# Optimization experiments

Measured on AMD Instinct MI355X. Metric: run time of the kernel, lower is better.

Reference implementation:

```python
import jax, jax.numpy as jnp
import numpy as np

N = 8192


def _bcsoftmax1d(x, c):
    # sort ascending by log(budget) - logit, as in the torch reference
    order = jnp.argsort(jnp.log(c) - x)
    xs, cs = x[order], c[order]
    # reversed log-cumsum-exp: log_r[i] = logsumexp(xs[i:])
    log_r = jnp.flip(jax.lax.cumlogsumexp(jnp.flip(xs)))
    # s[i] = 1 - sum_{j<i} cs[j]
    s = 1.0 - (jnp.cumsum(cs) - cs)
    in_kb = (cs == 0) | ((s - cs > 0) & (xs - log_r + jnp.log(s) > jnp.log(cs)))
    mask = ~in_kb
    m = jnp.max(jnp.where(mask, xs, -jnp.inf))
    exp_x = jnp.exp(xs - m)
    s2 = 1.0 - jnp.sum(cs * in_kb)
    r = jnp.sum(exp_x * mask)
    ys = jnp.where(mask, s2 * exp_x / r, cs)
    # undo the sort
    return jnp.zeros_like(ys).at[order].set(ys)


def setup_inputs() -> dict:
    key = jax.random.key(0)
    k1, k2, k3, k4 = jax.random.split(key, 4)
    x = jax.random.normal(k1, (N,), dtype=jnp.float32)
    # budgets must be > 0; scale so sum(c) ~ 1 so constraints can bind
    c = jax.random.uniform(k2, (N,), dtype=jnp.float32) * (2.0 / N)
    W = jax.random.normal(k3, (N, N), dtype=jnp.float32) / np.sqrt(N).astype(np.float32)
    b = jax.random.normal(k4, (N,), dtype=jnp.float32) * 0.01
    return {"x": x, "c": c, "W": W, "b": b}


def reference(x, c, W, b):
    h = W @ x + b  # nn.Linear: x @ W^T + b == W @ x for 1D x
    return _bcsoftmax1d(h, c)
```

## Files before the change

### kernel.cpp

```cpp
#include <hip/hip_runtime.h>
#include <math.h>

#define N 8192
typedef unsigned long long u64;

#define CE(a, b, d) do { if (((a) > (b)) == (d)) { u64 _t = (a); (a) = (b); (b) = _t; } } while (0)

__global__ __launch_bounds__(256) void matvec_k(const float* __restrict__ W,
                                                const float* __restrict__ x,
                                                const float* __restrict__ b,
                                                float* __restrict__ h) {
  const int lane = threadIdx.x & 63;
  const int row = blockIdx.x * 4 + (threadIdx.x >> 6);
  const float4* Wr = reinterpret_cast<const float4*>(W + (size_t)row * N);
  const float4* x4 = reinterpret_cast<const float4*>(x);
  float acc = 0.f;
#pragma unroll 8
  for (int k = 0; k < 32; ++k) {
    const int i = k * 64 + lane;
    const float4 w = Wr[i];
    const float4 xv = x4[i];
    acc = fmaf(w.x, xv.x, acc);
    acc = fmaf(w.y, xv.y, acc);
    acc = fmaf(w.z, xv.z, acc);
    acc = fmaf(w.w, xv.w, acc);
  }
#pragma unroll
  for (int off = 32; off > 0; off >>= 1) acc += __shfl_down(acc, off, 64);
  if (lane == 0) h[row] = acc + b[row];
}

__global__ __launch_bounds__(1024) void bcsoftmax_k(const float* __restrict__ h,
                                                    const float* __restrict__ c,
                                                    float* __restrict__ out) {
  __shared__ u64 sb[N];
  __shared__ float red[32];
  __shared__ float bcast[4];
  const int tid = threadIdx.x;
  const int lane = tid & 63;
  const int wid = tid >> 6;

  u64 v[8];

  float hv[8], cv[8];
  {
    const float4* h4 = reinterpret_cast<const float4*>(h);
    const float4* c4 = reinterpret_cast<const float4*>(c);
    const float4 a0 = h4[tid * 2], a1 = h4[tid * 2 + 1];
    const float4 b0 = c4[tid * 2], b1 = c4[tid * 2 + 1];
    hv[0] = a0.x; hv[1] = a0.y; hv[2] = a0.z; hv[3] = a0.w;
    hv[4] = a1.x; hv[5] = a1.y; hv[6] = a1.z; hv[7] = a1.w;
    cv[0] = b0.x; cv[1] = b0.y; cv[2] = b0.z; cv[3] = b0.w;
    cv[4] = b1.x; cv[5] = b1.y; cv[6] = b1.z; cv[7] = b1.w;
  }
  float lmax = -INFINITY;
#pragma unroll
  for (int p = 0; p < 8; ++p) {
    const int g = tid * 8 + p;
    const float key = logf(cv[p]) - hv[p];
    unsigned int u = __float_as_uint(key);
    u = (u & 0x80000000u) ? ~u : (u | 0x80000000u);
    v[p] = ((u64)u << 32) | (unsigned int)g;
    lmax = fmaxf(lmax, hv[p]);
  }
  CE(v[0], v[1], true); CE(v[2], v[3], false); CE(v[4], v[5], true); CE(v[6], v[7], false);
  CE(v[0], v[2], true); CE(v[1], v[3], true); CE(v[4], v[6], false); CE(v[5], v[7], false);
  CE(v[0], v[1], true); CE(v[2], v[3], true); CE(v[4], v[5], false); CE(v[6], v[7], false);
  {
    const bool d8 = ((tid & 1) == 0);
    CE(v[0], v[4], d8); CE(v[1], v[5], d8); CE(v[2], v[6], d8); CE(v[3], v[7], d8);
    CE(v[0], v[2], d8); CE(v[1], v[3], d8); CE(v[4], v[6], d8); CE(v[5], v[7], d8);
    CE(v[0], v[1], d8); CE(v[2], v[3], d8); CE(v[4], v[5], d8); CE(v[6], v[7], d8);
  }
#pragma unroll
  for (int p = 0; p < 8; ++p) sb[tid * 8 + p] = v[p];

#pragma unroll
  for (int off = 32; off > 0; off >>= 1) lmax = fmaxf(lmax, __shfl_down(lmax, off, 64));
  if (lane == 0) red[wid] = lmax;
  __syncthreads();
  if (tid == 0) {
    float mm = red[0];
    for (int i = 1; i < 16; ++i) mm = fmaxf(mm, red[i]);
    bcast[0] = mm;
  }

  for (int k = 16;; k <<= 1) {
    for (int j = k >> 1; j >= 8; j >>= 1) {
#pragma unroll
      for (int rep = 0; rep < 4; ++rep) {
        const int i = rep * 1024 + tid;
        const int t = ((i & ~(j - 1)) << 1) | (i & (j - 1));
        const int p = t | j;
        const u64 a = sb[t];
        const u64 bb = sb[p];
        const bool asc = ((t & k) == 0);
        if ((a > bb) == asc) { sb[t] = bb; sb[p] = a; }
      }
      __syncthreads();
    }
#pragma unroll
    for (int p = 0; p < 8; ++p) v[p] = sb[tid * 8 + p];
    const bool d = (((tid * 8) & k) == 0);
    CE(v[0], v[4], d); CE(v[1], v[5], d); CE(v[2], v[6], d); CE(v[3], v[7], d);
    CE(v[0], v[2], d); CE(v[1], v[3], d); CE(v[4], v[6], d); CE(v[5], v[7], d);
    CE(v[0], v[1], d); CE(v[2], v[3], d); CE(v[4], v[5], d); CE(v[6], v[7], d);
    if (k == N) break;
#pragma unroll
    for (int p = 0; p < 8; ++p) sb[tid * 8 + p] = v[p];
    __syncthreads();
  }

  const float M = bcast[0];
  int idx[8];
  float xs[8], cs[8], e[8];
  float cloc = 0.f, eloc = 0.f;
#pragma unroll
  for (int p = 0; p < 8; ++p) {
    const int id = (int)(v[p] & 0xFFFFFFFFull);
    idx[p] = id;
    xs[p] = h[id];
    cs[p] = c[id];
  }
#pragma unroll
  for (int p = 0; p < 8; ++p) {
    e[p] = expf(xs[p] - M);
    cloc += cs[p];
    eloc += e[p];
  }

  float cinc = cloc;
#pragma unroll
  for (int off = 1; off < 64; off <<= 1) {
    const float t = __shfl_up(cinc, off, 64);
    if (lane >= off) cinc += t;
  }
  float cwex = __shfl_up(cinc, 1, 64);
  if (lane == 0) cwex = 0.f;
  __syncthreads();
  if (lane == 63) red[wid] = cinc;
  __syncthreads();
  if (tid < 16) {
    float winc = red[tid];
#pragma unroll
    for (int off = 1; off < 16; off <<= 1) {
      const float t = __shfl_up(winc, off, 64);
      if (lane >= off) winc += t;
    }
    float wexc = __shfl_up(winc, 1, 64);
    if (tid == 0) wexc = 0.f;
    red[tid] = wexc;
  }
  __syncthreads();
  const float cthread_excl = red[wid] + cwex;

  float sinc = eloc;
#pragma unroll
  for (int off = 1; off < 64; off <<= 1) {
    const float t = __shfl_down(sinc, off, 64);
    if (lane + off < 64) sinc += t;
  }
  float swex = __shfl_down(sinc, 1, 64);
  if (lane == 63) swex = 0.f;
  __syncthreads();
  if (lane == 0) red[16 + wid] = sinc;
  __syncthreads();
  if (tid < 16) {
    float winc = red[16 + tid];
#pragma unroll
    for (int off = 1; off < 16; off <<= 1) {
      const float t = __shfl_down(winc, off, 64);
      if (tid + off < 16) winc += t;
    }
    float wexc = __shfl_down(winc, 1, 64);
    if (tid == 15) wexc = 0.f;
    red[16 + tid] = wexc;
  }
  __syncthreads();
  const float ethread_exsuf = red[16 + wid] + swex;

  float lsuf[8];
  lsuf[7] = e[7];
#pragma unroll
  for (int p = 6; p >= 0; --p) lsuf[p] = e[p] + lsuf[p + 1];
  float cexc = 0.f;
  bool kb[8];
  float lm = -INFINITY, lkbc = 0.f;
#pragma unroll
  for (int p = 0; p < 8; ++p) {
    const float s = 1.0f - (cthread_excl + cexc);
    const float suff = ethread_exsuf + lsuf[p];
    const float log_r = M + logf(suff);
    const bool in_kb =
        (cs[p] == 0.0f) ||
        ((s - cs[p] > 0.0f) && (xs[p] - log_r + logf(s) > logf(cs[p])));
    kb[p] = in_kb;
    if (in_kb) lkbc += cs[p];
    else       lm = fmaxf(lm, xs[p]);
    cexc += cs[p];
  }
#pragma unroll
  for (int off = 32; off > 0; off >>= 1) {
    lm = fmaxf(lm, __shfl_down(lm, off, 64));
    lkbc += __shfl_down(lkbc, off, 64);
  }
  __syncthreads();
  if (lane == 0) { red[wid] = lm; red[16 + wid] = lkbc; }
  __syncthreads();
  if (tid == 0) {
    float mm = red[0], sc = red[16];
    for (int i = 1; i < 16; ++i) { mm = fmaxf(mm, red[i]); sc += red[16 + i]; }
    bcast[1] = mm;
    bcast[2] = 1.0f - sc;
  }
  __syncthreads();
  const float m = bcast[1];
  const float s2 = bcast[2];

  float lr = 0.f;
#pragma unroll
  for (int p = 0; p < 8; ++p)
    if (!kb[p]) lr += expf(xs[p] - m);
#pragma unroll
  for (int off = 32; off > 0; off >>= 1) lr += __shfl_down(lr, off, 64);
  if (lane == 0) red[wid] = lr;
  __syncthreads();
  if (tid == 0) {
    float rr = red[0];
    for (int i = 1; i < 16; ++i) rr += red[i];
    bcast[3] = rr;
  }
  __syncthreads();
  const float r = bcast[3];

#pragma unroll
  for (int p = 0; p < 8; ++p) {
    out[idx[p]] = kb[p] ? cs[p] : s2 * expf(xs[p] - m) / r;
  }
}

extern "C" void kernel_launch(void* const* d_in, const int* in_sizes, int n_in,
                              void* d_out, int out_size, void* d_ws, size_t ws_size,
                              hipStream_t stream) {
  (void)in_sizes; (void)n_in; (void)out_size;
  const float* x = (const float*)d_in[0];
  const float* c = (const float*)d_in[1];
  const float* W = (const float*)d_in[2];
  const float* b = (const float*)d_in[3];
  float* out = (float*)d_out;
  float* h = (ws_size >= (size_t)N * sizeof(float)) ? (float*)d_ws : out;

  matvec_k<<<N / 4, 256, 0, stream>>>(W, x, b, h);
  bcsoftmax_k<<<1, 1024, 0, stream>>>(h, c, out);
}
```

Baseline: 420.3 us.

## Do in-wavefront bitonic stages with shuffles and stage gathers and scatters in LDS

```diff
diff --git a/kernel.cpp b/kernel.cpp
--- a/kernel.cpp
+++ b/kernel.cpp
@@ -34,6 +34,8 @@
                                                     const float* __restrict__ c,
                                                     float* __restrict__ out) {
   __shared__ u64 sb[N];
+  __shared__ float hbuf[N];
+  __shared__ float cbuf[N];
   __shared__ float red[32];
   __shared__ float bcast[4];
   const int tid = threadIdx.x;
@@ -48,6 +50,10 @@
     const float4* c4 = reinterpret_cast<const float4*>(c);
     const float4 a0 = h4[tid * 2], a1 = h4[tid * 2 + 1];
     const float4 b0 = c4[tid * 2], b1 = c4[tid * 2 + 1];
+    reinterpret_cast<float4*>(hbuf)[tid * 2]     = a0;
+    reinterpret_cast<float4*>(hbuf)[tid * 2 + 1] = a1;
+    reinterpret_cast<float4*>(cbuf)[tid * 2]     = b0;
+    reinterpret_cast<float4*>(cbuf)[tid * 2 + 1] = b1;
     hv[0] = a0.x; hv[1] = a0.y; hv[2] = a0.z; hv[3] = a0.w;
     hv[4] = a1.x; hv[5] = a1.y; hv[6] = a1.z; hv[7] = a1.w;
     cv[0] = b0.x; cv[1] = b0.y; cv[2] = b0.z; cv[3] = b0.w;
@@ -63,6 +69,10 @@
     v[p] = ((u64)u << 32) | (unsigned int)g;
     lmax = fmaxf(lmax, hv[p]);
   }
+#pragma unroll
+  for (int off = 32; off > 0; off >>= 1) lmax = fmaxf(lmax, __shfl_down(lmax, off, 64));
+  if (lane == 0) red[wid] = lmax;
+
   CE(v[0], v[1], true); CE(v[2], v[3], false); CE(v[4], v[5], true); CE(v[6], v[7], false);
   CE(v[0], v[2], true); CE(v[1], v[3], true); CE(v[4], v[6], false); CE(v[5], v[7], false);
   CE(v[0], v[1], true); CE(v[2], v[3], true); CE(v[4], v[5], false); CE(v[6], v[7], false);
@@ -72,43 +82,71 @@
     CE(v[0], v[2], d8); CE(v[1], v[3], d8); CE(v[4], v[6], d8); CE(v[5], v[7], d8);
     CE(v[0], v[1], d8); CE(v[2], v[3], d8); CE(v[4], v[5], d8); CE(v[6], v[7], d8);
   }
-#pragma unroll
-  for (int p = 0; p < 8; ++p) sb[tid * 8 + p] = v[p];
-
-#pragma unroll
-  for (int off = 32; off > 0; off >>= 1) lmax = fmaxf(lmax, __shfl_down(lmax, off, 64));
-  if (lane == 0) red[wid] = lmax;
-  __syncthreads();
-  if (tid == 0) {
-    float mm = red[0];
-    for (int i = 1; i < 16; ++i) mm = fmaxf(mm, red[i]);
-    bcast[0] = mm;
-  }
-
-  for (int k = 16;; k <<= 1) {
+
+  for (int k = 16; k <= 512; k <<= 1) {
+    const bool asc = (((tid * 8) & k) == 0);
     for (int j = k >> 1; j >= 8; j >>= 1) {
-#pragma unroll
-      for (int rep = 0; rep < 4; ++rep) {
-        const int i = rep * 1024 + tid;
-        const int t = ((i & ~(j - 1)) << 1) | (i & (j - 1));
-        const int p = t | j;
-        const u64 a = sb[t];
-        const u64 bb = sb[p];
+      const int d = j >> 3;
+      const bool keepmin = (((lane & d) == 0) == asc);
+#pragma unroll
+      for (int p = 0; p < 8; ++p) {
+        const u64 o = __shfl_xor(v[p], d, 64);
+        const bool take = keepmin ? (o < v[p]) : (o > v[p]);
+        if (take) v[p] = o;
+      }
+    }
+    CE(v[0], v[4], asc); CE(v[1], v[5], asc); CE(v[2], v[6], asc); CE(v[3], v[7], asc);
+    CE(v[0], v[2], asc); CE(v[1], v[3], asc); CE(v[4], v[6], asc); CE(v[5], v[7], asc);
+    CE(v[0], v[1], asc); CE(v[2], v[3], asc); CE(v[4], v[5], asc); CE(v[6], v[7], asc);
+  }
+
+  for (int k = 1024; k <= N; k <<= 1) {
+#pragma unroll
+    for (int p = 0; p < 8; p += 2) {
+      ulonglong2 t2; t2.x = v[p]; t2.y = v[p + 1];
+      *reinterpret_cast<ulonglong2*>(&sb[tid * 8 + p]) = t2;
+    }
+    __syncthreads();
+    if (k == 1024 && tid == 0) {
+      float mm = red[0];
+      for (int i = 1; i < 16; ++i) mm = fmaxf(mm, red[i]);
+      bcast[0] = mm;
+    }
+    for (int j = k >> 1; j >= 512; j >>= 1) {
+      const int jh = j >> 1;
+#pragma unroll
+      for (int rep = 0; rep < 2; ++rep) {
+        const int q = rep * 1024 + tid;
+        const int u = ((q & ~(jh - 1)) << 1) | (q & (jh - 1));
+        const int t = u * 2;
         const bool asc = ((t & k) == 0);
-        if ((a > bb) == asc) { sb[t] = bb; sb[p] = a; }
+        ulonglong2 A = *reinterpret_cast<ulonglong2*>(&sb[t]);
+        ulonglong2 B = *reinterpret_cast<ulonglong2*>(&sb[t + j]);
+        CE(A.x, B.x, asc); CE(A.y, B.y, asc);
+        *reinterpret_cast<ulonglong2*>(&sb[t]) = A;
+        *reinterpret_cast<ulonglong2*>(&sb[t + j]) = B;
       }
       __syncthreads();
     }
 #pragma unroll
-    for (int p = 0; p < 8; ++p) v[p] = sb[tid * 8 + p];
-    const bool d = (((tid * 8) & k) == 0);
-    CE(v[0], v[4], d); CE(v[1], v[5], d); CE(v[2], v[6], d); CE(v[3], v[7], d);
-    CE(v[0], v[2], d); CE(v[1], v[3], d); CE(v[4], v[6], d); CE(v[5], v[7], d);
-    CE(v[0], v[1], d); CE(v[2], v[3], d); CE(v[4], v[5], d); CE(v[6], v[7], d);
-    if (k == N) break;
-#pragma unroll
-    for (int p = 0; p < 8; ++p) sb[tid * 8 + p] = v[p];
-    __syncthreads();
+    for (int p = 0; p < 8; p += 2) {
+      const ulonglong2 t2 = *reinterpret_cast<ulonglong2*>(&sb[tid * 8 + p]);
+      v[p] = t2.x; v[p + 1] = t2.y;
+    }
+    const bool asc = (((tid * 8) & k) == 0);
+    for (int j = 256; j >= 8; j >>= 1) {
+      const int d = j >> 3;
+      const bool keepmin = (((lane & d) == 0) == asc);
+#pragma unroll
+      for (int p = 0; p < 8; ++p) {
+        const u64 o = __shfl_xor(v[p], d, 64);
+        const bool take = keepmin ? (o < v[p]) : (o > v[p]);
+        if (take) v[p] = o;
+      }
+    }
+    CE(v[0], v[4], asc); CE(v[1], v[5], asc); CE(v[2], v[6], asc); CE(v[3], v[7], asc);
+    CE(v[0], v[2], asc); CE(v[1], v[3], asc); CE(v[4], v[6], asc); CE(v[5], v[7], asc);
+    CE(v[0], v[1], asc); CE(v[2], v[3], asc); CE(v[4], v[5], asc); CE(v[6], v[7], asc);
   }
 
   const float M = bcast[0];
@@ -119,8 +157,8 @@
   for (int p = 0; p < 8; ++p) {
     const int id = (int)(v[p] & 0xFFFFFFFFull);
     idx[p] = id;
-    xs[p] = h[id];
-    cs[p] = c[id];
+    xs[p] = hbuf[id];
+    cs[p] = cbuf[id];
   }
 #pragma unroll
   for (int p = 0; p < 8; ++p) {
@@ -217,10 +255,13 @@
   const float m = bcast[1];
   const float s2 = bcast[2];
 
+  float ey[8];
   float lr = 0.f;
 #pragma unroll
-  for (int p = 0; p < 8; ++p)
-    if (!kb[p]) lr += expf(xs[p] - m);
+  for (int p = 0; p < 8; ++p) {
+    ey[p] = expf(xs[p] - m);
+    if (!kb[p]) lr += ey[p];
+  }
 #pragma unroll
   for (int off = 32; off > 0; off >>= 1) lr += __shfl_down(lr, off, 64);
   if (lane == 0) red[wid] = lr;
@@ -233,9 +274,17 @@
   __syncthreads();
   const float r = bcast[3];
 
-#pragma unroll
-  for (int p = 0; p < 8; ++p) {
-    out[idx[p]] = kb[p] ? cs[p] : s2 * expf(xs[p] - m) / r;
+  float* ybuf = hbuf;
+#pragma unroll
+  for (int p = 0; p < 8; ++p) {
+    ybuf[idx[p]] = kb[p] ? cs[p] : s2 * ey[p] / r;
+  }
+  __syncthreads();
+  {
+    const float4* y4 = reinterpret_cast<const float4*>(ybuf);
+    float4* o4 = reinterpret_cast<float4*>(out);
+    o4[tid * 2]     = y4[tid * 2];
+    o4[tid * 2 + 1] = y4[tid * 2 + 1];
   }
 }
 
```

After: 416.1 us. No clear change (-1.0%).

## Replace single-block bitonic sort with parallel rank-counting sort across many blocks

Applied to the files above, without the earlier changes.

```diff
diff --git a/kernel.cpp b/kernel.cpp
--- a/kernel.cpp
+++ b/kernel.cpp
@@ -3,13 +3,13 @@
 
 #define N 8192
 typedef unsigned long long u64;
-
-#define CE(a, b, d) do { if (((a) > (b)) == (d)) { u64 _t = (a); (a) = (b); (b) = _t; } } while (0)
 
 __global__ __launch_bounds__(256) void matvec_k(const float* __restrict__ W,
                                                 const float* __restrict__ x,
                                                 const float* __restrict__ b,
-                                                float* __restrict__ h) {
+                                                const float* __restrict__ c,
+                                                float* __restrict__ h,
+                                                u64* __restrict__ Kkey) {
   const int lane = threadIdx.x & 63;
   const int row = blockIdx.x * 4 + (threadIdx.x >> 6);
   const float4* Wr = reinterpret_cast<const float4*>(W + (size_t)row * N);
@@ -27,100 +27,87 @@
   }
 #pragma unroll
   for (int off = 32; off > 0; off >>= 1) acc += __shfl_down(acc, off, 64);
-  if (lane == 0) h[row] = acc + b[row];
+  if (lane == 0) {
+    const float hv = acc + b[row];
+    h[row] = hv;
+    const float key = logf(c[row]) - hv;
+    unsigned int u = __float_as_uint(key);
+    u = (u & 0x80000000u) ? ~u : (u | 0x80000000u);
+    Kkey[row] = ((u64)u << 13) | (unsigned int)row;
+  }
+}
+
+__global__ __launch_bounds__(256) void rank_k(const u64* __restrict__ Kkey,
+                                              unsigned int* __restrict__ partial) {
+  const int i = blockIdx.x * 256 + threadIdx.x;
+  const u64 Ki = Kkey[i];
+  const u64* __restrict__ Kc = Kkey + blockIdx.y * 1024;
+  unsigned int cnt = 0;
+#pragma unroll 8
+  for (int t = 0; t < 1024; ++t) cnt += (Kc[t] < Ki) ? 1u : 0u;
+  partial[blockIdx.y * N + i] = cnt;
 }
 
 __global__ __launch_bounds__(1024) void bcsoftmax_k(const float* __restrict__ h,
                                                     const float* __restrict__ c,
+                                                    const unsigned int* __restrict__ partial,
                                                     float* __restrict__ out) {
-  __shared__ u64 sb[N];
+  __shared__ float hbuf[N];
+  __shared__ float cbuf[N];
+  __shared__ unsigned int sperm[N];
   __shared__ float red[32];
   __shared__ float bcast[4];
   const int tid = threadIdx.x;
   const int lane = tid & 63;
   const int wid = tid >> 6;
 
-  u64 v[8];
-
-  float hv[8], cv[8];
+  float lmax = -INFINITY;
   {
     const float4* h4 = reinterpret_cast<const float4*>(h);
     const float4* c4 = reinterpret_cast<const float4*>(c);
     const float4 a0 = h4[tid * 2], a1 = h4[tid * 2 + 1];
     const float4 b0 = c4[tid * 2], b1 = c4[tid * 2 + 1];
-    hv[0] = a0.x; hv[1] = a0.y; hv[2] = a0.z; hv[3] = a0.w;
-    hv[4] = a1.x; hv[5] = a1.y; hv[6] = a1.z; hv[7] = a1.w;
-    cv[0] = b0.x; cv[1] = b0.y; cv[2] = b0.z; cv[3] = b0.w;
-    cv[4] = b1.x; cv[5] = b1.y; cv[6] = b1.z; cv[7] = b1.w;
-  }
-  float lmax = -INFINITY;
-#pragma unroll
-  for (int p = 0; p < 8; ++p) {
-    const int g = tid * 8 + p;
-    const float key = logf(cv[p]) - hv[p];
-    unsigned int u = __float_as_uint(key);
-    u = (u & 0x80000000u) ? ~u : (u | 0x80000000u);
-    v[p] = ((u64)u << 32) | (unsigned int)g;
-    lmax = fmaxf(lmax, hv[p]);
-  }
-  CE(v[0], v[1], true); CE(v[2], v[3], false); CE(v[4], v[5], true); CE(v[6], v[7], false);
-  CE(v[0], v[2], true); CE(v[1], v[3], true); CE(v[4], v[6], false); CE(v[5], v[7], false);
-  CE(v[0], v[1], true); CE(v[2], v[3], true); CE(v[4], v[5], false); CE(v[6], v[7], false);
-  {
-    const bool d8 = ((tid & 1) == 0);
-    CE(v[0], v[4], d8); CE(v[1], v[5], d8); CE(v[2], v[6], d8); CE(v[3], v[7], d8);
-    CE(v[0], v[2], d8); CE(v[1], v[3], d8); CE(v[4], v[6], d8); CE(v[5], v[7], d8);
-    CE(v[0], v[1], d8); CE(v[2], v[3], d8); CE(v[4], v[5], d8); CE(v[6], v[7], d8);
-  }
-#pragma unroll
-  for (int p = 0; p < 8; ++p) sb[tid * 8 + p] = v[p];
-
+    reinterpret_cast<float4*>(hbuf)[tid * 2]     = a0;
+    reinterpret_cast<float4*>(hbuf)[tid * 2 + 1] = a1;
+    reinterpret_cast<float4*>(cbuf)[tid * 2]     = b0;
+    reinterpret_cast<float4*>(cbuf)[tid * 2 + 1] = b1;
+    lmax = fmaxf(lmax, fmaxf(fmaxf(a0.x, a0.y), fmaxf(a0.z, a0.w)));
+    lmax = fmaxf(lmax, fmaxf(fmaxf(a1.x, a1.y), fmaxf(a1.z, a1.w)));
+  }
 #pragma unroll
   for (int off = 32; off > 0; off >>= 1) lmax = fmaxf(lmax, __shfl_down(lmax, off, 64));
   if (lane == 0) red[wid] = lmax;
+
+#pragma unroll
+  for (int p = 0; p < 8; ++p) {
+    const int g = p * 1024 + tid;
+    unsigned int rank = 0;
+#pragma unroll
+    for (int y = 0; y < 8; ++y) rank += partial[y * N + g];
+    sperm[rank] = (unsigned int)g;
+  }
   __syncthreads();
   if (tid == 0) {
     float mm = red[0];
     for (int i = 1; i < 16; ++i) mm = fmaxf(mm, red[i]);
     bcast[0] = mm;
   }
-
-  for (int k = 16;; k <<= 1) {
-    for (int j = k >> 1; j >= 8; j >>= 1) {
-#pragma unroll
-      for (int rep = 0; rep < 4; ++rep) {
-        const int i = rep * 1024 + tid;
-        const int t = ((i & ~(j - 1)) << 1) | (i & (j - 1));
-        const int p = t | j;
-        const u64 a = sb[t];
-        const u64 bb = sb[p];
-        const bool asc = ((t & k) == 0);
-        if ((a > bb) == asc) { sb[t] = bb; sb[p] = a; }
-      }
-      __syncthreads();
-    }
-#pragma unroll
-    for (int p = 0; p < 8; ++p) v[p] = sb[tid * 8 + p];
-    const bool d = (((tid * 8) & k) == 0);
-    CE(v[0], v[4], d); CE(v[1], v[5], d); CE(v[2], v[6], d); CE(v[3], v[7], d);
-    CE(v[0], v[2], d); CE(v[1], v[3], d); CE(v[4], v[6], d); CE(v[5], v[7], d);
-    CE(v[0], v[1], d); CE(v[2], v[3], d); CE(v[4], v[5], d); CE(v[6], v[7], d);
-    if (k == N) break;
-#pragma unroll
-    for (int p = 0; p < 8; ++p) sb[tid * 8 + p] = v[p];
-    __syncthreads();
-  }
-
+  __syncthreads();
   const float M = bcast[0];
+
   int idx[8];
   float xs[8], cs[8], e[8];
   float cloc = 0.f, eloc = 0.f;
-#pragma unroll
-  for (int p = 0; p < 8; ++p) {
-    const int id = (int)(v[p] & 0xFFFFFFFFull);
-    idx[p] = id;
-    xs[p] = h[id];
-    cs[p] = c[id];
+  {
+    const uint4* sp4 = reinterpret_cast<const uint4*>(sperm);
+    const uint4 i0 = sp4[tid * 2], i1 = sp4[tid * 2 + 1];
+    idx[0] = i0.x; idx[1] = i0.y; idx[2] = i0.z; idx[3] = i0.w;
+    idx[4] = i1.x; idx[5] = i1.y; idx[6] = i1.z; idx[7] = i1.w;
+  }
+#pragma unroll
+  for (int p = 0; p < 8; ++p) {
+    xs[p] = hbuf[idx[p]];
+    cs[p] = cbuf[idx[p]];
   }
 #pragma unroll
   for (int p = 0; p < 8; ++p) {
@@ -217,10 +204,13 @@
   const float m = bcast[1];
   const float s2 = bcast[2];
 
+  float ey[8];
   float lr = 0.f;
 #pragma unroll
-  for (int p = 0; p < 8; ++p)
-    if (!kb[p]) lr += expf(xs[p] - m);
+  for (int p = 0; p < 8; ++p) {
+    ey[p] = expf(xs[p] - m);
+    if (!kb[p]) lr += ey[p];
+  }
 #pragma unroll
   for (int off = 32; off > 0; off >>= 1) lr += __shfl_down(lr, off, 64);
   if (lane == 0) red[wid] = lr;
@@ -233,23 +223,36 @@
   __syncthreads();
   const float r = bcast[3];
 
-#pragma unroll
-  for (int p = 0; p < 8; ++p) {
-    out[idx[p]] = kb[p] ? cs[p] : s2 * expf(xs[p] - m) / r;
+  float* ybuf = hbuf;
+#pragma unroll
+  for (int p = 0; p < 8; ++p) {
+    ybuf[idx[p]] = kb[p] ? cs[p] : s2 * ey[p] / r;
+  }
+  __syncthreads();
+  {
+    const float4* y4 = reinterpret_cast<const float4*>(ybuf);
+    float4* o4 = reinterpret_cast<float4*>(out);
+    o4[tid * 2]     = y4[tid * 2];
+    o4[tid * 2 + 1] = y4[tid * 2 + 1];
   }
 }
 
 extern "C" void kernel_launch(void* const* d_in, const int* in_sizes, int n_in,
                               void* d_out, int out_size, void* d_ws, size_t ws_size,
                               hipStream_t stream) {
-  (void)in_sizes; (void)n_in; (void)out_size;
+  (void)in_sizes; (void)n_in; (void)out_size; (void)ws_size;
   const float* x = (const float*)d_in[0];
   const float* c = (const float*)d_in[1];
   const float* W = (const float*)d_in[2];
   const float* b = (const float*)d_in[3];
   float* out = (float*)d_out;
-  float* h = (ws_size >= (size_t)N * sizeof(float)) ? (float*)d_ws : out;
-
-  matvec_k<<<N / 4, 256, 0, stream>>>(W, x, b, h);
-  bcsoftmax_k<<<1, 1024, 0, stream>>>(h, c, out);
-}
+
+  char* ws = (char*)d_ws;
+  float* h = (float*)ws;
+  u64* Kkey = (u64*)(ws + 32768);
+  unsigned int* partial = (unsigned int*)(ws + 32768 + 65536);
+
+  matvec_k<<<N / 4, 256, 0, stream>>>(W, x, b, c, h, Kkey);
+  rank_k<<<dim3(32, 8), 256, 0, stream>>>(Kkey, partial);
+  bcsoftmax_k<<<1, 1024, 0, stream>>>(h, c, partial, out);
+}
```

Result: faster. 409.2 us (-2.6%).
